# Optimization experiments

Hardware: AMD Instinct MI355X
Metric: run time of the kernel (lower is better)

The kernel has to match this reference:

```python
import jax, jax.numpy as jnp
import numpy as np

HIDDEN = 128
NUM_BASIS = 50
NUM_FILTERS = 128
CUTOFF = 10.0
N_NODES = 20000
N_EDGES = 640000
LOG2 = 0.6931471805599453


def ssp(x):
    # ShiftedSoftplus: softplus(x) - log(2)
    return jax.nn.softplus(x) - LOG2


def setup_inputs() -> dict:
    key = jax.random.key(0)
    ks = jax.random.split(key, 10)
    def xavier(k, shape):
        fan_in, fan_out = shape[0], shape[1]
        a = jnp.sqrt(6.0 / (fan_in + fan_out))
        return jax.random.uniform(k, shape, jnp.float32, -a, a)
    x = jax.random.normal(ks[0], (N_NODES, HIDDEN), jnp.float32)
    edge_index = jax.random.randint(ks[1], (2, N_EDGES), 0, N_NODES, jnp.int64)
    edge_weight = jax.random.uniform(ks[2], (N_EDGES,), jnp.float32) * CUTOFF
    edge_attr = jax.random.normal(ks[3], (N_EDGES, NUM_BASIS), jnp.float32)
    return {
        "x": x,
        "edge_index": edge_index,
        "edge_weight": edge_weight,
        "edge_attr": edge_attr,
        "mlp_w1": xavier(ks[4], (NUM_BASIS, NUM_FILTERS)),
        "mlp_b1": jnp.zeros((NUM_FILTERS,), jnp.float32),
        "mlp_w2": xavier(ks[5], (NUM_FILTERS, NUM_FILTERS)),
        "mlp_b2": jnp.zeros((NUM_FILTERS,), jnp.float32),
        "lin1_w": xavier(ks[6], (HIDDEN, NUM_FILTERS)),
        "lin2_w": xavier(ks[7], (NUM_FILTERS, HIDDEN)),
        "lin2_b": jnp.zeros((HIDDEN,), jnp.float32),
        "lin_w": xavier(ks[8], (HIDDEN, HIDDEN)),
        "lin_b": jnp.zeros((HIDDEN,), jnp.float32),
    }


def reference(x, edge_index, edge_weight, edge_attr,
              mlp_w1, mlp_b1, mlp_w2, mlp_b2,
              lin1_w, lin2_w, lin2_b, lin_w, lin_b):
    src, dst = edge_index[0], edge_index[1]
    # cosine cutoff on edge distance  [E]
    C = 0.5 * (jnp.cos(edge_weight * (jnp.pi / CUTOFF)) + 1.0)
    # filter MLP on expanded basis  [E, F]
    W = ssp(edge_attr @ mlp_w1 + mlp_b1) @ mlp_w2 + mlp_b2
    W = W * C[:, None]
    # CFConv: gather source node features, weight, scatter-add to targets
    h = x @ lin1_w                      # [N, F]
    msg = h[src] * W                    # [E, F]
    agg = jax.ops.segment_sum(msg, dst, num_segments=N_NODES)  # [N, F]
    h = agg @ lin2_w + lin2_b           # [N, H]
    # interaction block tail
    h = ssp(h)
    out = h @ lin_w + lin_b             # [N, H]
    return out
```

## Files before the change

kernel.cpp:

```cpp
#include <hip/hip_runtime.h>
#include <hip/hip_bf16.h>

#define NNODES 20000
#define NEDGES 640000
#define NB 50
#define NF 128

typedef unsigned int uint_t;
typedef unsigned short ushort_t;

typedef __bf16 bf16x8 __attribute__((ext_vector_type(8)));
typedef float f32x4 __attribute__((ext_vector_type(4)));

__device__ __forceinline__ uint_t f2bf(float f) {
    uint_t u = __float_as_uint(f);
    return (u + 0x7fffu + ((u >> 16) & 1u)) >> 16;
}

__device__ __forceinline__ float ssp_f(float x) {
    float t = __expf(-fabsf(x));
    return fmaxf(x, 0.0f) + __logf(1.0f + t) - 0.6931471805599453f;
}

__global__ __launch_bounds__(256) void k_zero(float4* __restrict__ p) {
    int i = blockIdx.x * 256 + threadIdx.x;
    p[i] = make_float4(0.f, 0.f, 0.f, 0.f);
}

__global__ __launch_bounds__(256) void k_node1(const float* __restrict__ X,
                                               const float* __restrict__ W,
                                               float* __restrict__ Y, int nrows)
{
    __shared__ alignas(16) ushort_t sx[64 * 136];
    const int tid  = threadIdx.x;
    const int wv   = tid >> 6, lane = tid & 63;
    const int col  = lane & 15, quad = lane >> 4;

    bf16x8 wf[2][4];
    #pragma unroll
    for (int nt = 0; nt < 2; ++nt) {
        int n = wv * 32 + nt * 16 + col;
        #pragma unroll
        for (int kc = 0; kc < 4; ++kc)
            #pragma unroll
            for (int j = 0; j < 8; ++j)
                wf[nt][kc][j] = (__bf16)W[(kc * 32 + quad * 8 + j) * NF + n];
    }

    const int rbase = blockIdx.x * 64;
    for (int i = tid; i < 64 * 64; i += 256) {
        int r = i >> 6, c = i & 63;
        int gr = rbase + r;
        float2 v = (gr < nrows) ? *reinterpret_cast<const float2*>(&X[(size_t)gr * NF + 2 * c])
                                : make_float2(0.f, 0.f);
        reinterpret_cast<uint_t*>(sx)[r * 68 + c] = f2bf(v.x) | (f2bf(v.y) << 16);
    }
    __syncthreads();

    f32x4 acc[4][2] = {};
    #pragma unroll
    for (int kc = 0; kc < 4; ++kc) {
        bf16x8 af[4];
        #pragma unroll
        for (int mt = 0; mt < 4; ++mt)
            af[mt] = *reinterpret_cast<const bf16x8*>(&sx[(mt * 16 + col) * 136 + kc * 32 + quad * 8]);
        #pragma unroll
        for (int mt = 0; mt < 4; ++mt)
            #pragma unroll
            for (int nt = 0; nt < 2; ++nt)
                acc[mt][nt] = __builtin_amdgcn_mfma_f32_16x16x32_bf16(af[mt], wf[nt][kc], acc[mt][nt], 0, 0, 0);
    }
    #pragma unroll
    for (int mt = 0; mt < 4; ++mt)
        #pragma unroll
        for (int nt = 0; nt < 2; ++nt)
            #pragma unroll
            for (int r = 0; r < 4; ++r) {
                int row = rbase + mt * 16 + quad * 4 + r;
                if (row < nrows) Y[(size_t)row * NF + wv * 32 + nt * 16 + col] = acc[mt][nt][r];
            }
}

__global__ __launch_bounds__(256) void k_tail(const float* __restrict__ X,
                                              const float* __restrict__ W1, const float* __restrict__ B1,
                                              const float* __restrict__ W2, const float* __restrict__ B2,
                                              float* __restrict__ Y, int nrows)
{
    __shared__ alignas(16) ushort_t sx[64 * 136];
    __shared__ alignas(16) ushort_t st[64 * 136];
    const int tid  = threadIdx.x;
    const int wv   = tid >> 6, lane = tid & 63;
    const int col  = lane & 15, quad = lane >> 4;

    bf16x8 wf1[2][4], wf2[2][4];
    float rb1[2], rb2[2];
    #pragma unroll
    for (int nt = 0; nt < 2; ++nt) {
        int n = wv * 32 + nt * 16 + col;
        rb1[nt] = B1[n]; rb2[nt] = B2[n];
        #pragma unroll
        for (int kc = 0; kc < 4; ++kc)
            #pragma unroll
            for (int j = 0; j < 8; ++j) {
                int k = kc * 32 + quad * 8 + j;
                wf1[nt][kc][j] = (__bf16)W1[k * NF + n];
                wf2[nt][kc][j] = (__bf16)W2[k * NF + n];
            }
    }

    const int rbase = blockIdx.x * 64;
    for (int i = tid; i < 64 * 64; i += 256) {
        int r = i >> 6, c = i & 63;
        int gr = rbase + r;
        float2 v = (gr < nrows) ? *reinterpret_cast<const float2*>(&X[(size_t)gr * NF + 2 * c])
                                : make_float2(0.f, 0.f);
        reinterpret_cast<uint_t*>(sx)[r * 68 + c] = f2bf(v.x) | (f2bf(v.y) << 16);
    }
    __syncthreads();

    f32x4 acc[4][2];
    #pragma unroll
    for (int mt = 0; mt < 4; ++mt)
        #pragma unroll
        for (int nt = 0; nt < 2; ++nt)
            acc[mt][nt] = f32x4{rb1[nt], rb1[nt], rb1[nt], rb1[nt]};
    #pragma unroll
    for (int kc = 0; kc < 4; ++kc) {
        bf16x8 af[4];
        #pragma unroll
        for (int mt = 0; mt < 4; ++mt)
            af[mt] = *reinterpret_cast<const bf16x8*>(&sx[(mt * 16 + col) * 136 + kc * 32 + quad * 8]);
        #pragma unroll
        for (int mt = 0; mt < 4; ++mt)
            #pragma unroll
            for (int nt = 0; nt < 2; ++nt)
                acc[mt][nt] = __builtin_amdgcn_mfma_f32_16x16x32_bf16(af[mt], wf1[nt][kc], acc[mt][nt], 0, 0, 0);
    }
    #pragma unroll
    for (int mt = 0; mt < 4; ++mt)
        #pragma unroll
        for (int nt = 0; nt < 2; ++nt)
            #pragma unroll
            for (int r = 0; r < 4; ++r)
                st[(mt * 16 + quad * 4 + r) * 136 + wv * 32 + nt * 16 + col] =
                    (ushort_t)f2bf(ssp_f(acc[mt][nt][r]));
    __syncthreads();

    f32x4 acc2[4][2];
    #pragma unroll
    for (int mt = 0; mt < 4; ++mt)
        #pragma unroll
        for (int nt = 0; nt < 2; ++nt)
            acc2[mt][nt] = f32x4{rb2[nt], rb2[nt], rb2[nt], rb2[nt]};
    #pragma unroll
    for (int kc = 0; kc < 4; ++kc) {
        bf16x8 af[4];
        #pragma unroll
        for (int mt = 0; mt < 4; ++mt)
            af[mt] = *reinterpret_cast<const bf16x8*>(&st[(mt * 16 + col) * 136 + kc * 32 + quad * 8]);
        #pragma unroll
        for (int mt = 0; mt < 4; ++mt)
            #pragma unroll
            for (int nt = 0; nt < 2; ++nt)
                acc2[mt][nt] = __builtin_amdgcn_mfma_f32_16x16x32_bf16(af[mt], wf2[nt][kc], acc2[mt][nt], 0, 0, 0);
    }
    #pragma unroll
    for (int mt = 0; mt < 4; ++mt)
        #pragma unroll
        for (int nt = 0; nt < 2; ++nt)
            #pragma unroll
            for (int r = 0; r < 4; ++r) {
                int row = rbase + mt * 16 + quad * 4 + r;
                if (row < nrows) Y[(size_t)row * NF + wv * 32 + nt * 16 + col] = acc2[mt][nt][r];
            }
}

__global__ __launch_bounds__(256) void k_edge(
    const int* __restrict__ esrc, const int* __restrict__ edst,
    const float* __restrict__ ew, const float* __restrict__ ea,
    const float* __restrict__ w1, const float* __restrict__ b1,
    const float* __restrict__ w2, const float* __restrict__ b2,
    const float* __restrict__ h, float* __restrict__ agg)
{
    __shared__ alignas(16) ushort_t sea[32 * 72];
    __shared__ alignas(16) ushort_t st1[32 * 136];
    __shared__ float sC[32];
    __shared__ int ssrc[32], sdst[32];

    const int tid  = threadIdx.x;
    const int wv   = tid >> 6, lane = tid & 63;
    const int col  = lane & 15, quad = lane >> 4;

    for (int i = tid; i < 32 * 72; i += 256) sea[i] = 0;

    bf16x8 w1f[2][2];
    bf16x8 w2f[2][4];
    float rb1[2], rb2[2];
    #pragma unroll
    for (int nt = 0; nt < 2; ++nt) {
        int n = wv * 32 + nt * 16 + col;
        rb1[nt] = b1[n]; rb2[nt] = b2[n];
        #pragma unroll
        for (int kc = 0; kc < 2; ++kc)
            #pragma unroll
            for (int j = 0; j < 8; ++j) {
                int k = kc * 32 + quad * 8 + j;
                w1f[nt][kc][j] = (__bf16)((k < NB) ? w1[k * NF + n] : 0.0f);
            }
        #pragma unroll
        for (int kc = 0; kc < 4; ++kc)
            #pragma unroll
            for (int j = 0; j < 8; ++j)
                w2f[nt][kc][j] = (__bf16)w2[(kc * 32 + quad * 8 + j) * NF + n];
    }

    const int e0 = blockIdx.x * 320;

    for (int it = 0; it < 10; ++it) {
        const int ebase = e0 + it * 32;
        __syncthreads();
        for (int i = tid; i < 32 * NB; i += 256) {
            int e = i / NB;
            int k = i - e * NB;
            sea[e * 72 + k] = (ushort_t)f2bf(ea[(size_t)ebase * NB + i]);
        }
        if (tid < 32) {
            int e = ebase + tid;
            ssrc[tid] = esrc[e];
            sdst[tid] = edst[e];
            sC[tid]   = 0.5f * (cosf(ew[e] * 0.31415926535897931f) + 1.0f);
        }
        __syncthreads();

        float hg[2][2][4];
        #pragma unroll
        for (int mt = 0; mt < 2; ++mt)
            #pragma unroll
            for (int nt = 0; nt < 2; ++nt)
                #pragma unroll
                for (int r = 0; r < 4; ++r) {
                    int ml = mt * 16 + quad * 4 + r;
                    hg[mt][nt][r] = h[(size_t)ssrc[ml] * NF + wv * 32 + nt * 16 + col];
                }

        f32x4 acc1[2][2];
        #pragma unroll
        for (int mt = 0; mt < 2; ++mt)
            #pragma unroll
            for (int nt = 0; nt < 2; ++nt)
                acc1[mt][nt] = f32x4{rb1[nt], rb1[nt], rb1[nt], rb1[nt]};
        #pragma unroll
        for (int kc = 0; kc < 2; ++kc) {
            bf16x8 af[2];
            #pragma unroll
            for (int mt = 0; mt < 2; ++mt)
                af[mt] = *reinterpret_cast<const bf16x8*>(&sea[(mt * 16 + col) * 72 + kc * 32 + quad * 8]);
            #pragma unroll
            for (int mt = 0; mt < 2; ++mt)
                #pragma unroll
                for (int nt = 0; nt < 2; ++nt)
                    acc1[mt][nt] = __builtin_amdgcn_mfma_f32_16x16x32_bf16(af[mt], w1f[nt][kc], acc1[mt][nt], 0, 0, 0);
        }
        #pragma unroll
        for (int mt = 0; mt < 2; ++mt)
            #pragma unroll
            for (int nt = 0; nt < 2; ++nt)
                #pragma unroll
                for (int r = 0; r < 4; ++r)
                    st1[(mt * 16 + quad * 4 + r) * 136 + wv * 32 + nt * 16 + col] =
                        (ushort_t)f2bf(ssp_f(acc1[mt][nt][r]));
        __syncthreads();

        f32x4 acc2[2][2];
        #pragma unroll
        for (int mt = 0; mt < 2; ++mt)
            #pragma unroll
            for (int nt = 0; nt < 2; ++nt)
                acc2[mt][nt] = f32x4{rb2[nt], rb2[nt], rb2[nt], rb2[nt]};
        #pragma unroll
        for (int kc = 0; kc < 4; ++kc) {
            bf16x8 af[2];
            #pragma unroll
            for (int mt = 0; mt < 2; ++mt)
                af[mt] = *reinterpret_cast<const bf16x8*>(&st1[(mt * 16 + col) * 136 + kc * 32 + quad * 8]);
            #pragma unroll
            for (int mt = 0; mt < 2; ++mt)
                #pragma unroll
                for (int nt = 0; nt < 2; ++nt)
                    acc2[mt][nt] = __builtin_amdgcn_mfma_f32_16x16x32_bf16(af[mt], w2f[nt][kc], acc2[mt][nt], 0, 0, 0);
        }
        #pragma unroll
        for (int mt = 0; mt < 2; ++mt)
            #pragma unroll
            for (int nt = 0; nt < 2; ++nt)
                #pragma unroll
                for (int r = 0; r < 4; ++r) {
                    int ml = mt * 16 + quad * 4 + r;
                    float val = acc2[mt][nt][r] * sC[ml];
                    atomicAdd(&agg[(size_t)sdst[ml] * NF + wv * 32 + nt * 16 + col], val * hg[mt][nt][r]);
                }
    }
}

extern "C" void kernel_launch(void* const* d_in, const int* in_sizes, int n_in,
                              void* d_out, int out_size, void* d_ws, size_t ws_size,
                              hipStream_t stream) {
    const float* x    = (const float*)d_in[0];
    const int*   eidx = (const int*)d_in[1];
    const float* ew   = (const float*)d_in[2];
    const float* ea   = (const float*)d_in[3];
    const float* w1   = (const float*)d_in[4];
    const float* b1   = (const float*)d_in[5];
    const float* w2   = (const float*)d_in[6];
    const float* b2   = (const float*)d_in[7];
    const float* l1w  = (const float*)d_in[8];
    const float* l2w  = (const float*)d_in[9];
    const float* l2b  = (const float*)d_in[10];
    const float* lw   = (const float*)d_in[11];
    const float* lb   = (const float*)d_in[12];
    (void)in_sizes; (void)n_in; (void)out_size; (void)ws_size;

    float* h   = (float*)d_ws;
    float* agg = (float*)((char*)d_ws + (size_t)NNODES * NF * 4);

    hipLaunchKernelGGL(k_zero, dim3(2500), dim3(256), 0, stream, (float4*)agg);
    hipLaunchKernelGGL(k_node1, dim3(313), dim3(256), 0, stream, x, l1w, h, NNODES);
    hipLaunchKernelGGL(k_edge, dim3(2000), dim3(256), 0, stream,
                       eidx, eidx + NEDGES, ew, ea, w1, b1, w2, b2, h, agg);
    hipLaunchKernelGGL(k_tail, dim3(313), dim3(256), 0, stream,
                       agg, l2w, l2b, lw, lb, (float*)d_out, NNODES);
}
```

Baseline: 587.9 us.

## Give each wave its own edge tile in edge kernel, weights in LDS

Restructures the edge filter kernel so each wave processes an independent 16-edge tile across all 128 filters. Weights are pre-swizzled into shared memory as MFMA fragments instead of held in registers. Edge attributes are loaded straight from global into A fragments, and the hidden layer is staged in a per-wave LDS buffer, which removes block-wide __syncthreads from the inner loop. The trade-offs are more LDS traffic for the B fragments, more registers for the gathered h values and accumulators, uncoalesced float2 loads of edge_attr, and a switch to the faster but less accurate __cosf.

```diff
diff --git a/kernel.cpp b/kernel.cpp
--- a/kernel.cpp
+++ b/kernel.cpp
@@ -182,123 +182,116 @@
     const float* __restrict__ w2, const float* __restrict__ b2,
     const float* __restrict__ h, float* __restrict__ agg)
 {
-    __shared__ alignas(16) ushort_t sea[32 * 72];
-    __shared__ alignas(16) ushort_t st1[32 * 136];
-    __shared__ float sC[32];
-    __shared__ int ssrc[32], sdst[32];
+    __shared__ alignas(16) ushort_t w1f[16 * 64 * 8];
+    __shared__ alignas(16) ushort_t w2f[32 * 64 * 8];
+    __shared__ alignas(16) ushort_t st1[4][16 * 72];
 
     const int tid  = threadIdx.x;
     const int wv   = tid >> 6, lane = tid & 63;
     const int col  = lane & 15, quad = lane >> 4;
 
-    for (int i = tid; i < 32 * 72; i += 256) sea[i] = 0;
-
-    bf16x8 w1f[2][2];
-    bf16x8 w2f[2][4];
-    float rb1[2], rb2[2];
-    #pragma unroll
-    for (int nt = 0; nt < 2; ++nt) {
-        int n = wv * 32 + nt * 16 + col;
-        rb1[nt] = b1[n]; rb2[nt] = b2[n];
-        #pragma unroll
-        for (int kc = 0; kc < 2; ++kc)
-            #pragma unroll
-            for (int j = 0; j < 8; ++j) {
-                int k = kc * 32 + quad * 8 + j;
-                w1f[nt][kc][j] = (__bf16)((k < NB) ? w1[k * NF + n] : 0.0f);
-            }
-        #pragma unroll
-        for (int kc = 0; kc < 4; ++kc)
-            #pragma unroll
-            for (int j = 0; j < 8; ++j)
-                w2f[nt][kc][j] = (__bf16)w2[(kc * 32 + quad * 8 + j) * NF + n];
-    }
-
-    const int e0 = blockIdx.x * 320;
-
-    for (int it = 0; it < 10; ++it) {
-        const int ebase = e0 + it * 32;
-        __syncthreads();
-        for (int i = tid; i < 32 * NB; i += 256) {
-            int e = i / NB;
-            int k = i - e * NB;
-            sea[e * 72 + k] = (ushort_t)f2bf(ea[(size_t)ebase * NB + i]);
-        }
-        if (tid < 32) {
-            int e = ebase + tid;
-            ssrc[tid] = esrc[e];
-            sdst[tid] = edst[e];
-            sC[tid]   = 0.5f * (cosf(ew[e] * 0.31415926535897931f) + 1.0f);
-        }
-        __syncthreads();
-
-        float hg[2][2][4];
-        #pragma unroll
-        for (int mt = 0; mt < 2; ++mt)
-            #pragma unroll
-            for (int nt = 0; nt < 2; ++nt)
-                #pragma unroll
-                for (int r = 0; r < 4; ++r) {
-                    int ml = mt * 16 + quad * 4 + r;
-                    hg[mt][nt][r] = h[(size_t)ssrc[ml] * NF + wv * 32 + nt * 16 + col];
-                }
-
-        f32x4 acc1[2][2];
-        #pragma unroll
-        for (int mt = 0; mt < 2; ++mt)
-            #pragma unroll
-            for (int nt = 0; nt < 2; ++nt)
-                acc1[mt][nt] = f32x4{rb1[nt], rb1[nt], rb1[nt], rb1[nt]};
-        #pragma unroll
-        for (int kc = 0; kc < 2; ++kc) {
-            bf16x8 af[2];
-            #pragma unroll
-            for (int mt = 0; mt < 2; ++mt)
-                af[mt] = *reinterpret_cast<const bf16x8*>(&sea[(mt * 16 + col) * 72 + kc * 32 + quad * 8]);
-            #pragma unroll
-            for (int mt = 0; mt < 2; ++mt)
-                #pragma unroll
-                for (int nt = 0; nt < 2; ++nt)
-                    acc1[mt][nt] = __builtin_amdgcn_mfma_f32_16x16x32_bf16(af[mt], w1f[nt][kc], acc1[mt][nt], 0, 0, 0);
-        }
-        #pragma unroll
-        for (int mt = 0; mt < 2; ++mt)
-            #pragma unroll
-            for (int nt = 0; nt < 2; ++nt)
+    for (int idx = tid; idx < 16 * 64; idx += 256) {
+        int fr = idx >> 6, l = idx & 63;
+        int ntg = fr >> 1, kc = fr & 1;
+        int n = ntg * 16 + (l & 15), kb = kc * 32 + (l >> 4) * 8;
+        ushort_t* d = &w1f[idx * 8];
+        #pragma unroll
+        for (int j = 0; j < 8; ++j) {
+            int k = kb + j;
+            d[j] = (ushort_t)((k < NB) ? f2bf(w1[k * NF + n]) : 0u);
+        }
+    }
+    for (int idx = tid; idx < 32 * 64; idx += 256) {
+        int fr = idx >> 6, l = idx & 63;
+        int ntg = fr >> 2, kc = fr & 3;
+        int n = ntg * 16 + (l & 15), kb = kc * 32 + (l >> 4) * 8;
+        ushort_t* d = &w2f[idx * 8];
+        #pragma unroll
+        for (int j = 0; j < 8; ++j)
+            d[j] = (ushort_t)f2bf(w2[(kb + j) * NF + n]);
+    }
+    float rb1[8], rb2[8];
+    #pragma unroll
+    for (int nt = 0; nt < 8; ++nt) { rb1[nt] = b1[nt * 16 + col]; rb2[nt] = b2[nt * 16 + col]; }
+    __syncthreads();
+
+    ushort_t* myst = st1[wv];
+
+    for (int it = 0; it < 5; ++it) {
+        const int ebase = blockIdx.x * 320 + wv * 80 + it * 16;
+
+        int srcv[4], dstv[4];
+        float Cw[4];
+        #pragma unroll
+        for (int r = 0; r < 4; ++r) {
+            int e = ebase + quad * 4 + r;
+            srcv[r] = esrc[e];
+            dstv[r] = edst[e];
+            Cw[r]   = 0.5f * (__cosf(ew[e] * 0.31415926535897931f) + 1.0f);
+        }
+
+        float hg[8][4];
+        #pragma unroll
+        for (int nt = 0; nt < 8; ++nt)
+            #pragma unroll
+            for (int r = 0; r < 4; ++r)
+                hg[nt][r] = h[(size_t)srcv[r] * NF + nt * 16 + col];
+
+        const float* erow = ea + (size_t)(ebase + col) * NB;
+        bf16x8 af0, af1;
+        #pragma unroll
+        for (int p = 0; p < 4; ++p) {
+            float2 v = *reinterpret_cast<const float2*>(erow + quad * 8 + 2 * p);
+            af0[2 * p]     = (__bf16)v.x;
+            af0[2 * p + 1] = (__bf16)v.y;
+        }
+        #pragma unroll
+        for (int p = 0; p < 4; ++p) {
+            int k = 32 + quad * 8 + 2 * p;
+            float2 v = (k + 2 <= NB) ? *reinterpret_cast<const float2*>(erow + k)
+                                     : make_float2(0.f, 0.f);
+            af1[2 * p]     = (__bf16)v.x;
+            af1[2 * p + 1] = (__bf16)v.y;
+        }
+
+        f32x4 acc2[8];
+        #pragma unroll
+        for (int nt = 0; nt < 8; ++nt) acc2[nt] = f32x4{rb2[nt], rb2[nt], rb2[nt], rb2[nt]};
+
+        #pragma unroll
+        for (int hf = 0; hf < 2; ++hf) {
+            f32x4 acc1[4];
+            #pragma unroll
+            for (int nt = 0; nt < 4; ++nt) {
+                int ntg = hf * 4 + nt;
+                acc1[nt] = f32x4{rb1[ntg], rb1[ntg], rb1[ntg], rb1[ntg]};
+                bf16x8 bw0 = *reinterpret_cast<const bf16x8*>(&w1f[((ntg * 2 + 0) * 64 + lane) * 8]);
+                bf16x8 bw1 = *reinterpret_cast<const bf16x8*>(&w1f[((ntg * 2 + 1) * 64 + lane) * 8]);
+                acc1[nt] = __builtin_amdgcn_mfma_f32_16x16x32_bf16(af0, bw0, acc1[nt], 0, 0, 0);
+                acc1[nt] = __builtin_amdgcn_mfma_f32_16x16x32_bf16(af1, bw1, acc1[nt], 0, 0, 0);
+            }
+            #pragma unroll
+            for (int nt = 0; nt < 4; ++nt)
                 #pragma unroll
                 for (int r = 0; r < 4; ++r)
-                    st1[(mt * 16 + quad * 4 + r) * 136 + wv * 32 + nt * 16 + col] =
-                        (ushort_t)f2bf(ssp_f(acc1[mt][nt][r]));
-        __syncthreads();
-
-        f32x4 acc2[2][2];
-        #pragma unroll
-        for (int mt = 0; mt < 2; ++mt)
-            #pragma unroll
-            for (int nt = 0; nt < 2; ++nt)
-                acc2[mt][nt] = f32x4{rb2[nt], rb2[nt], rb2[nt], rb2[nt]};
-        #pragma unroll
-        for (int kc = 0; kc < 4; ++kc) {
-            bf16x8 af[2];
-            #pragma unroll
-            for (int mt = 0; mt < 2; ++mt)
-                af[mt] = *reinterpret_cast<const bf16x8*>(&st1[(mt * 16 + col) * 136 + kc * 32 + quad * 8]);
-            #pragma unroll
-            for (int mt = 0; mt < 2; ++mt)
-                #pragma unroll
-                for (int nt = 0; nt < 2; ++nt)
-                    acc2[mt][nt] = __builtin_amdgcn_mfma_f32_16x16x32_bf16(af[mt], w2f[nt][kc], acc2[mt][nt], 0, 0, 0);
-        }
-        #pragma unroll
-        for (int mt = 0; mt < 2; ++mt)
-            #pragma unroll
-            for (int nt = 0; nt < 2; ++nt)
-                #pragma unroll
-                for (int r = 0; r < 4; ++r) {
-                    int ml = mt * 16 + quad * 4 + r;
-                    float val = acc2[mt][nt][r] * sC[ml];
-                    atomicAdd(&agg[(size_t)sdst[ml] * NF + wv * 32 + nt * 16 + col], val * hg[mt][nt][r]);
-                }
+                    myst[(quad * 4 + r) * 72 + nt * 16 + col] = (ushort_t)f2bf(ssp_f(acc1[nt][r]));
+            bf16x8 a20 = *reinterpret_cast<const bf16x8*>(&myst[col * 72 + 0 * 32 + quad * 8]);
+            bf16x8 a21 = *reinterpret_cast<const bf16x8*>(&myst[col * 72 + 1 * 32 + quad * 8]);
+            #pragma unroll
+            for (int nt = 0; nt < 8; ++nt) {
+                bf16x8 b20 = *reinterpret_cast<const bf16x8*>(&w2f[((nt * 4 + hf * 2 + 0) * 64 + lane) * 8]);
+                bf16x8 b21 = *reinterpret_cast<const bf16x8*>(&w2f[((nt * 4 + hf * 2 + 1) * 64 + lane) * 8]);
+                acc2[nt] = __builtin_amdgcn_mfma_f32_16x16x32_bf16(a20, b20, acc2[nt], 0, 0, 0);
+                acc2[nt] = __builtin_amdgcn_mfma_f32_16x16x32_bf16(a21, b21, acc2[nt], 0, 0, 0);
+            }
+        }
+
+        #pragma unroll
+        for (int nt = 0; nt < 8; ++nt)
+            #pragma unroll
+            for (int r = 0; r < 4; ++r)
+                atomicAdd(&agg[(size_t)dstv[r] * NF + nt * 16 + col],
+                          acc2[nt][r] * Cw[r] * hg[nt][r]);
     }
 }
 
```

Result: no change. 591.9 us (+0.7%).
